# Kernel tuning notes

Measured on AMD Instinct MI355X. Metric: run time of the kernel, lower is better.

## Reference

```python
import jax, jax.numpy as jnp
import numpy as np

N_NODES = 50000
N_EDGES = 800000
DIM = 128
LN_EPS = 1e-5


def setup_inputs() -> dict:
    key = jax.random.key(0)
    k1, k2, k3, k4 = jax.random.split(key, 4)
    h = jax.random.normal(k1, (N_NODES, DIM), dtype=jnp.float32)
    edge_index = jax.random.randint(k2, (2, N_EDGES), 0, N_NODES, dtype=jnp.int64)
    W = jax.random.normal(k3, (DIM, DIM), dtype=jnp.float32) / np.sqrt(DIM)
    b = jnp.zeros((DIM,), dtype=jnp.float32)
    gamma = jnp.ones((DIM,), dtype=jnp.float32)
    beta = jnp.zeros((DIM,), dtype=jnp.float32)
    t = jnp.zeros((), dtype=jnp.float32)
    return {"t": t, "h": h, "edge_index": edge_index, "batch_size": N_NODES,
            "W": W, "b": b, "gamma": gamma, "beta": beta}


def _gcn_conv(h, edge_index, W, b):
    """PyG-style GCNConv: D^{-1/2} (A+I) D^{-1/2} (h W) + b."""
    N = h.shape[0]
    loops = jnp.arange(N, dtype=edge_index.dtype)
    src = jnp.concatenate([edge_index[0], loops])  # [E+N]
    dst = jnp.concatenate([edge_index[1], loops])  # [E+N]
    # degree (with self loops) on destination nodes
    deg = jax.ops.segment_sum(jnp.ones_like(dst, dtype=h.dtype), dst, num_segments=N)
    dinv = jnp.where(deg > 0, jax.lax.rsqrt(deg), 0.0)
    norm = dinv[src] * dinv[dst]                    # [E+N]
    xw = h @ W                                      # [N, D]
    msg = xw[src] * norm[:, None]                   # gather + scale, [E+N, D]
    agg = jax.ops.segment_sum(msg, dst, num_segments=N)  # scatter-add, [N, D]
    return agg + b


def reference(t, h, edge_index, batch_size, W, b, gamma, beta):
    if h.ndim == 1:
        h = h[None, :]
    dh = _gcn_conv(h, edge_index, W, b)
    # LayerNorm over feature dim, then tanh
    mean = jnp.mean(dh, axis=-1, keepdims=True)
    var = jnp.mean(jnp.square(dh - mean), axis=-1, keepdims=True)
    dh = (dh - mean) * jax.lax.rsqrt(var + LN_EPS) * gamma + beta
    dh = jnp.tanh(dh)
    return (dh, jnp.zeros_like(edge_index), jnp.zeros_like(jnp.asarray(batch_size)))
```

## Files before the change

kernel.cpp:

```cpp
#include <hip/hip_runtime.h>
#include <math.h>

#define NN 50000
#define NE 800000
#define D  128
#define CNT_BLOCKS 1564
#define GEMM_BLOCKS 782
#define NROLES 2346
#define SC_BLOCKS 782

typedef __attribute__((ext_vector_type(8))) short bf16x8;
typedef __attribute__((ext_vector_type(4))) float f32x4;

__device__ __forceinline__ unsigned short f32_to_bf16(float f) {
    unsigned u = __float_as_uint(f);
    u = u + 0x7FFFu + ((u >> 16) & 1u);
    return (unsigned short)(u >> 16);
}

__device__ __forceinline__ float fast_tanh(float x) {
    float e = __expf(2.0f * x);
    return fmaf(-2.0f, __builtin_amdgcn_rcpf(e + 1.0f), 1.0f);
}

#define GLD16(P, VO, BASE)                                              \
    asm volatile(                                                       \
        "global_load_dword %0, %16, %32\n\t"                            \
        "global_load_dword %1, %17, %32\n\t"                            \
        "global_load_dword %2, %18, %32\n\t"                            \
        "global_load_dword %3, %19, %32\n\t"                            \
        "global_load_dword %4, %20, %32\n\t"                            \
        "global_load_dword %5, %21, %32\n\t"                            \
        "global_load_dword %6, %22, %32\n\t"                            \
        "global_load_dword %7, %23, %32\n\t"                            \
        "global_load_dword %8, %24, %32\n\t"                            \
        "global_load_dword %9, %25, %32\n\t"                            \
        "global_load_dword %10, %26, %32\n\t"                           \
        "global_load_dword %11, %27, %32\n\t"                           \
        "global_load_dword %12, %28, %32\n\t"                           \
        "global_load_dword %13, %29, %32\n\t"                           \
        "global_load_dword %14, %30, %32\n\t"                           \
        "global_load_dword %15, %31, %32\n\t"                           \
        "s_waitcnt vmcnt(0)"                                            \
        : "=&v"(P[0]),  "=&v"(P[1]),  "=&v"(P[2]),  "=&v"(P[3]),        \
          "=&v"(P[4]),  "=&v"(P[5]),  "=&v"(P[6]),  "=&v"(P[7]),        \
          "=&v"(P[8]),  "=&v"(P[9]),  "=&v"(P[10]), "=&v"(P[11]),       \
          "=&v"(P[12]), "=&v"(P[13]), "=&v"(P[14]), "=&v"(P[15])        \
        : "v"(VO[0]),  "v"(VO[1]),  "v"(VO[2]),  "v"(VO[3]),            \
          "v"(VO[4]),  "v"(VO[5]),  "v"(VO[6]),  "v"(VO[7]),            \
          "v"(VO[8]),  "v"(VO[9]),  "v"(VO[10]), "v"(VO[11]),           \
          "v"(VO[12]), "v"(VO[13]), "v"(VO[14]), "v"(VO[15]),           \
          "s"(BASE))

__global__ __launch_bounds__(256) void k_init(
        const float* __restrict__ Wg, int* __restrict__ deg,
        unsigned short* __restrict__ wpk, unsigned short* __restrict__ zb) {
    int tid = threadIdx.x;
    int idx = blockIdx.x * 256 + tid;

    if (idx < NN / 4) ((int4*)deg)[idx] = (int4){0, 0, 0, 0};

    if (blockIdx.x == 0) {
#pragma unroll 8
        for (int i = 0; i < 64; i++) {
            int o = i * 256 + tid;
            int j = o & 7, frag = o >> 3;
            int lo = frag & 15, quad = (frag >> 4) & 3;
            int kt = (frag >> 6) & 3, nt = frag >> 8;
            wpk[o] = f32_to_bf16(Wg[(kt * 32 + quad * 8 + j) * 128 + nt * 16 + lo]);
        }
    }
    if (blockIdx.x == 1 && tid < 64)
        ((unsigned*)(zb + (size_t)NN * D))[tid] = 0u;
}

__global__ __launch_bounds__(256) void k_count_gemm(
        const float* __restrict__ h, const uint4* __restrict__ wpk4,
        const int* __restrict__ ei, int* __restrict__ deg,
        int* __restrict__ ell, float* __restrict__ zf,
        int* __restrict__ outtail, int tailN) {
    int tid = threadIdx.x;
    int bid = blockIdx.x;

    {
        int gt = bid * 256 + tid;
        int tail4 = tailN >> 2;
        for (int i = gt; i < tail4; i += NROLES * 256)
            ((int4*)outtail)[i] = (int4){0, 0, 0, 0};
        if (gt == 0)
            for (int k2 = tail4 << 2; k2 < tailN; k2++) outtail[k2] = 0;
    }

    int rem = bid % 3;
    if (rem != 2) {
        int cnt = 2 * (bid / 3) + rem;
        int g = cnt * 256 + tid;
        if (g < NE / 2) {
            int2 s2 = ((const int2*)ei)[g];
            int2 d2 = ((const int2*)(ei + NE))[g];
            int r0 = atomicAdd(&deg[d2.x], 1);
            int r1 = atomicAdd(&deg[d2.y], 1);
            if (r0 < 64) ell[(size_t)d2.x * 64 + r0] = s2.x;
            if (r1 < 64) ell[(size_t)d2.y * 64 + r1] = s2.y;
        }
        return;
    }

    int gid = bid / 3;
    int w = tid >> 6, lane = tid & 63;
    int quad = lane >> 4, lo = lane & 15;
    int rowBase = gid * 64 + w * 16;
    int rowA = rowBase + lo; if (rowA > NN - 1) rowA = NN - 1;
    const float4* h4 = (const float4*)h;

    bf16x8 af[4];
#pragma unroll
    for (int kt = 0; kt < 4; kt++) {
        float4 u = h4[(size_t)rowA * 32 + kt * 8 + quad * 2];
        float4 v = h4[(size_t)rowA * 32 + kt * 8 + quad * 2 + 1];
        bf16x8 a;
        a[0] = (short)f32_to_bf16(u.x); a[1] = (short)f32_to_bf16(u.y);
        a[2] = (short)f32_to_bf16(u.z); a[3] = (short)f32_to_bf16(u.w);
        a[4] = (short)f32_to_bf16(v.x); a[5] = (short)f32_to_bf16(v.y);
        a[6] = (short)f32_to_bf16(v.z); a[7] = (short)f32_to_bf16(v.w);
        af[kt] = a;
    }

    f32x4 acc[8];
#pragma unroll
    for (int nt = 0; nt < 8; nt++) acc[nt] = (f32x4){0.f, 0.f, 0.f, 0.f};

#pragma unroll
    for (int kt = 0; kt < 4; kt++)
#pragma unroll
        for (int nt = 0; nt < 8; nt++) {
            uint4 tb = wpk4[nt * 256 + kt * 64 + lane];
            acc[nt] = __builtin_amdgcn_mfma_f32_16x16x32_bf16(
                af[kt], __builtin_bit_cast(bf16x8, tb), acc[nt], 0, 0, 0);
        }

#pragma unroll
    for (int reg = 0; reg < 4; reg++) {
        int row = rowBase + quad * 4 + reg;
        if (row < NN) {
#pragma unroll
            for (int nt = 0; nt < 8; nt++)
                zf[(size_t)row * D + nt * 16 + lo] = acc[nt][reg];
        }
    }
}

__global__ __launch_bounds__(256) void k_scale(
        const int* __restrict__ deg, const float* __restrict__ zf,
        unsigned short* __restrict__ zb) {
    int g = blockIdx.x * 256 + threadIdx.x;
    if (g < NN * 4) {
        int row = g >> 2, seg = g & 3;
        float dn = rsqrtf((float)deg[row] + 1.0f);
        const float4* src = (const float4*)(zf + (size_t)row * D + seg * 32);
        uint4* dst = (uint4*)(zb + (size_t)row * D + seg * 32);
#pragma unroll
        for (int i = 0; i < 4; i++) {
            float4 a = src[i * 2], bb = src[i * 2 + 1];
            uint4 o;
            o.x = (unsigned)f32_to_bf16(a.x * dn) | ((unsigned)f32_to_bf16(a.y * dn) << 16);
            o.y = (unsigned)f32_to_bf16(a.z * dn) | ((unsigned)f32_to_bf16(a.w * dn) << 16);
            o.z = (unsigned)f32_to_bf16(bb.x * dn) | ((unsigned)f32_to_bf16(bb.y * dn) << 16);
            o.w = (unsigned)f32_to_bf16(bb.z * dn) | ((unsigned)f32_to_bf16(bb.w * dn) << 16);
            dst[i] = o;
        }
    }
}

__global__ __launch_bounds__(256) void k_gather_ln(
        const int* __restrict__ deg, const int* __restrict__ ell,
        const unsigned* __restrict__ zbu,
        const float* __restrict__ bias, const float* __restrict__ gamma,
        const float* __restrict__ beta, float* __restrict__ out) {
    int tid = threadIdx.x;
    int w = tid >> 6, lane = tid & 63;
    int rowBase = blockIdx.x * 16 + w * 4;
    unsigned lane4 = (unsigned)(lane << 2);

    int m0[4]; float dn[4]; unsigned selfz[4]; int v[4];
#pragma unroll
    for (int r = 0; r < 4; r++) {
        int row = rowBase + r;
        int dg = __builtin_amdgcn_readfirstlane(deg[row]);
        dn[r] = rsqrtf((float)dg + 1.0f);
        m0[r] = (dg > 64) ? 64 : dg;
        selfz[r] = zbu[(size_t)row * 64 + lane];
        int t0 = ell[(size_t)row * 64 + lane];
        v[r] = (lane < m0[r]) ? t0 : NN;
    }

    float ax[4], ay[4];
#pragma unroll
    for (int r = 0; r < 4; r++) {
        ax[r] = __uint_as_float(selfz[r] << 16);
        ay[r] = __uint_as_float(selfz[r] & 0xFFFF0000u);
    }

    float2 x[4];
#pragma unroll
    for (int r = 0; r < 4; r++) {
        int nb = (m0[r] + 15) >> 4;
        for (int jb = 0; jb < nb; ++jb) {
            int j = jb << 4;
            unsigned vo[16], p[16];
#pragma unroll
            for (int q = 0; q < 16; q++) {
                int sq = __builtin_amdgcn_readlane(v[r], j + q);
                vo[q] = ((unsigned)sq << 8) + lane4;
            }
            GLD16(p, vo, zbu);
#pragma unroll
            for (int q = 0; q < 16; q++) {
                ax[r] += __uint_as_float(p[q] << 16);
                ay[r] += __uint_as_float(p[q] & 0xFFFF0000u);
            }
        }
        x[r].x = ax[r] * dn[r];
        x[r].y = ay[r] * dn[r];
    }

    float2 bi = ((const float2*)bias)[lane];
    float2 ga = ((const float2*)gamma)[lane];
    float2 be = ((const float2*)beta)[lane];
#pragma unroll
    for (int r = 0; r < 4; r++) {
        int row = rowBase + r;
        float y0 = x[r].x + bi.x;
        float y1 = x[r].y + bi.y;
        float s = y0 + y1;
#pragma unroll
        for (int off = 32; off > 0; off >>= 1) s += __shfl_xor(s, off, 64);
        float m = s * (1.0f / 128.0f);
        float v0f = y0 - m, v1f = y1 - m;
        float vs = v0f * v0f + v1f * v1f;
#pragma unroll
        for (int off = 32; off > 0; off >>= 1) vs += __shfl_xor(vs, off, 64);
        float rstd = rsqrtf(vs * (1.0f / 128.0f) + 1e-5f);
        float2 o;
        o.x = fast_tanh(v0f * rstd * ga.x + be.x);
        o.y = fast_tanh(v1f * rstd * ga.y + be.y);
        *(float2*)&out[(size_t)row * D + lane * 2] = o;
    }
}

extern "C" void kernel_launch(void* const* d_in, const int* in_sizes, int n_in,
                              void* d_out, int out_size, void* d_ws, size_t ws_size,
                              hipStream_t stream) {
    const float* h     = (const float*)d_in[1];
    const int*   ei    = (const int*)  d_in[2];
    const float* Wg    = (const float*)d_in[4];
    const float* b     = (const float*)d_in[5];
    const float* gamma = (const float*)d_in[6];
    const float* beta  = (const float*)d_in[7];
    float* out = (float*)d_out;

    char* wsb = (char*)d_ws;
    unsigned short* wpk = (unsigned short*)(wsb);
    int*            deg = (int*)(wsb + 32768);
    int*            ell = (int*)(wsb + 232768);
    unsigned short* zb  = (unsigned short*)(wsb + 13032768);
    float*          zf  = (float*)(wsb + 25833024);

    int tailN = out_size - NN * D;
    int* outtail = (int*)(out + (size_t)NN * D);

    k_init       <<<64,        256, 0, stream>>>(Wg, deg, wpk, zb);
    k_count_gemm <<<NROLES,    256, 0, stream>>>(h, (const uint4*)wpk, ei, deg, ell, zf, outtail, tailN);
    k_scale      <<<SC_BLOCKS, 256, 0, stream>>>(deg, zf, zb);
    k_gather_ln  <<<NN / 16,   256, 0, stream>>>(deg, ell, (const unsigned*)zb, b, gamma, beta, out);
}
```

Baseline: 195.1 us.

## Split count from GEMM and fuse degree scaling into the GEMM epilogue

The combined count+GEMM kernel is split into a standalone edge-count kernel and a GEMM kernel that runs after it. Because degrees are now final when the GEMM runs, the GEMM applies the rsqrt degree scale and bf16 conversion in its epilogue and writes zb directly. This drops the fp32 zf intermediate and the separate k_scale pass. In exchange the count and GEMM work no longer overlap inside one launch, and the count kernel now handles one edge per thread instead of two.

Measured after the change: 188.5 us. -3.4%, faster.

```diff
diff --git a/kernel.cpp b/kernel.cpp
--- a/kernel.cpp
+++ b/kernel.cpp
@@ -4,10 +4,8 @@
 #define NN 50000
 #define NE 800000
 #define D  128
-#define CNT_BLOCKS 1564
+#define CNT_BLOCKS 3125
 #define GEMM_BLOCKS 782
-#define NROLES 2346
-#define SC_BLOCKS 782
 
 typedef __attribute__((ext_vector_type(8))) short bf16x8;
 typedef __attribute__((ext_vector_type(4))) float f32x4;
@@ -74,39 +72,30 @@
         ((unsigned*)(zb + (size_t)NN * D))[tid] = 0u;
 }
 
-__global__ __launch_bounds__(256) void k_count_gemm(
+__global__ __launch_bounds__(256) void k_count(
+        const int* __restrict__ ei, int* __restrict__ deg,
+        int* __restrict__ ell, int* __restrict__ outtail, int tailN) {
+    int g = blockIdx.x * 256 + threadIdx.x;
+
+    {
+        int tail4 = tailN >> 2;
+        for (int i = g; i < tail4; i += CNT_BLOCKS * 256)
+            ((int4*)outtail)[i] = (int4){0, 0, 0, 0};
+        if (g == 0)
+            for (int k2 = tail4 << 2; k2 < tailN; k2++) outtail[k2] = 0;
+    }
+
+    int s = ei[g];
+    int d = ei[NE + g];
+    int r = atomicAdd(&deg[d], 1);
+    if (r < 64) ell[(size_t)d * 64 + r] = s;
+}
+
+__global__ __launch_bounds__(256) void k_gemm_scale(
         const float* __restrict__ h, const uint4* __restrict__ wpk4,
-        const int* __restrict__ ei, int* __restrict__ deg,
-        int* __restrict__ ell, float* __restrict__ zf,
-        int* __restrict__ outtail, int tailN) {
+        const int* __restrict__ deg, unsigned short* __restrict__ zb) {
     int tid = threadIdx.x;
-    int bid = blockIdx.x;
-
-    {
-        int gt = bid * 256 + tid;
-        int tail4 = tailN >> 2;
-        for (int i = gt; i < tail4; i += NROLES * 256)
-            ((int4*)outtail)[i] = (int4){0, 0, 0, 0};
-        if (gt == 0)
-            for (int k2 = tail4 << 2; k2 < tailN; k2++) outtail[k2] = 0;
-    }
-
-    int rem = bid % 3;
-    if (rem != 2) {
-        int cnt = 2 * (bid / 3) + rem;
-        int g = cnt * 256 + tid;
-        if (g < NE / 2) {
-            int2 s2 = ((const int2*)ei)[g];
-            int2 d2 = ((const int2*)(ei + NE))[g];
-            int r0 = atomicAdd(&deg[d2.x], 1);
-            int r1 = atomicAdd(&deg[d2.y], 1);
-            if (r0 < 64) ell[(size_t)d2.x * 64 + r0] = s2.x;
-            if (r1 < 64) ell[(size_t)d2.y * 64 + r1] = s2.y;
-        }
-        return;
-    }
-
-    int gid = bid / 3;
+    int gid = blockIdx.x;
     int w = tid >> 6, lane = tid & 63;
     int quad = lane >> 4, lo = lane & 15;
     int rowBase = gid * 64 + w * 16;
@@ -143,31 +132,10 @@
     for (int reg = 0; reg < 4; reg++) {
         int row = rowBase + quad * 4 + reg;
         if (row < NN) {
+            float dn = rsqrtf((float)deg[row] + 1.0f);
 #pragma unroll
             for (int nt = 0; nt < 8; nt++)
-                zf[(size_t)row * D + nt * 16 + lo] = acc[nt][reg];
-        }
-    }
-}
-
-__global__ __launch_bounds__(256) void k_scale(
-        const int* __restrict__ deg, const float* __restrict__ zf,
-        unsigned short* __restrict__ zb) {
-    int g = blockIdx.x * 256 + threadIdx.x;
-    if (g < NN * 4) {
-        int row = g >> 2, seg = g & 3;
-        float dn = rsqrtf((float)deg[row] + 1.0f);
-        const float4* src = (const float4*)(zf + (size_t)row * D + seg * 32);
-        uint4* dst = (uint4*)(zb + (size_t)row * D + seg * 32);
-#pragma unroll
-        for (int i = 0; i < 4; i++) {
-            float4 a = src[i * 2], bb = src[i * 2 + 1];
-            uint4 o;
-            o.x = (unsigned)f32_to_bf16(a.x * dn) | ((unsigned)f32_to_bf16(a.y * dn) << 16);
-            o.y = (unsigned)f32_to_bf16(a.z * dn) | ((unsigned)f32_to_bf16(a.w * dn) << 16);
-            o.z = (unsigned)f32_to_bf16(bb.x * dn) | ((unsigned)f32_to_bf16(bb.y * dn) << 16);
-            o.w = (unsigned)f32_to_bf16(bb.z * dn) | ((unsigned)f32_to_bf16(bb.w * dn) << 16);
-            dst[i] = o;
+                zb[(size_t)row * D + nt * 16 + lo] = f32_to_bf16(acc[nt][reg] * dn);
         }
     }
 }
@@ -264,13 +232,12 @@
     int*            deg = (int*)(wsb + 32768);
     int*            ell = (int*)(wsb + 232768);
     unsigned short* zb  = (unsigned short*)(wsb + 13032768);
-    float*          zf  = (float*)(wsb + 25833024);
 
     int tailN = out_size - NN * D;
     int* outtail = (int*)(out + (size_t)NN * D);
 
-    k_init       <<<64,        256, 0, stream>>>(Wg, deg, wpk, zb);
-    k_count_gemm <<<NROLES,    256, 0, stream>>>(h, (const uint4*)wpk, ei, deg, ell, zf, outtail, tailN);
-    k_scale      <<<SC_BLOCKS, 256, 0, stream>>>(deg, zf, zb);
-    k_gather_ln  <<<NN / 16,   256, 0, stream>>>(deg, ell, (const unsigned*)zb, b, gamma, beta, out);
-}
+    k_init       <<<64,          256, 0, stream>>>(Wg, deg, wpk, zb);
+    k_count      <<<CNT_BLOCKS,  256, 0, stream>>>(ei, deg, ell, outtail, tailN);
+    k_gemm_scale <<<GEMM_BLOCKS, 256, 0, stream>>>(h, (const uint4*)wpk, deg, zb);
+    k_gather_ln  <<<NN / 16,     256, 0, stream>>>(deg, ell, (const unsigned*)zb, b, gamma, beta, out);
+}
```
